# Optimization experiments

Hardware: AMD Instinct MI355X
Metric: run time of the kernel (lower is better)

## Reference

```python
import jax, jax.numpy as jnp
import numpy as np

N, B, L = 1000, 16, 12
H, IN_DIM, OUT_DIM, E = 64, 3, 1, 16000


def _gru_cell(x, h, Wi, Wh, bi, bh):
    # torch nn.GRU gate order: r, z, n
    gi = x @ Wi.T + bi
    gh = h @ Wh.T + bh
    ir, iz, inn = jnp.split(gi, 3, axis=-1)
    hr, hz, hn = jnp.split(gh, 3, axis=-1)
    r = jax.nn.sigmoid(ir + hr)
    z = jax.nn.sigmoid(iz + hz)
    n = jnp.tanh(inn + r * hn)
    return (1.0 - z) * n + z * h


def setup_inputs():
    key = jax.random.key(0)
    ks = jax.random.split(key, 24)
    def rn(k, shape, s=0.1):
        return jax.random.normal(k, shape, dtype=jnp.float32) * s
    return {
        "hidden0": rn(ks[0], (N, B, H), 1.0),
        "hidden1": rn(ks[1], (N, B, H), 1.0),
        "features": rn(ks[2], (N, H), 1.0),
        "labels": rn(ks[3], (N, B, L, IN_DIM), 1.0),
        "edge_index": jax.random.randint(ks[4], (2, E), 0, N),
        # GRU1: input_dim -> H
        "Wi1": rn(ks[5], (3 * H, IN_DIM)), "Wh1": rn(ks[6], (3 * H, H)),
        "bi1": rn(ks[7], (3 * H,)), "bh1": rn(ks[8], (3 * H,)),
        # MetaGAT MLP: 2H -> 16 -> 2 -> 2H*H
        "W1": rn(ks[9], (16, 2 * H)), "b1": rn(ks[10], (16,)),
        "W2": rn(ks[11], (2, 16)), "b2": rn(ks[12], (2,)),
        "W3": rn(ks[13], (2 * H * H, 2)), "b3": rn(ks[14], (2 * H * H,)),
        # GRU2: H -> H
        "Wi2": rn(ks[15], (3 * H, H)), "Wh2": rn(ks[16], (3 * H, H)),
        "bi2": rn(ks[17], (3 * H,)), "bh2": rn(ks[18], (3 * H,)),
        # output layer: 2H -> OUT_DIM
        "Wo": rn(ks[19], (OUT_DIM, 2 * H)), "bo": rn(ks[20], (OUT_DIM,)),
    }


def reference(hidden0, hidden1, features, labels, edge_index,
              Wi1, Wh1, bi1, bh1, W1, b1, W2, b2, W3, b3,
              Wi2, Wh2, bi2, bh2, Wo, bo):
    n, b, length, _ = labels.shape
    h = Wh1.shape[1]
    out_dim = Wo.shape[0]
    in_dim = Wi1.shape[1]
    aux = labels[..., out_dim:]  # [N,B,L,aux_dim]
    # add self loops (as in MetaGAT.forward)
    loops = jnp.arange(n)
    src = jnp.concatenate([edge_index[0], loops])  # j, source
    dst = jnp.concatenate([edge_index[1], loops])  # i, target
    # per-edge weight matrices; features are constant across timesteps so hoist
    ft = jnp.concatenate([features[dst], features[src]], axis=-1)  # [Etot,2H]
    w = jax.nn.sigmoid(ft @ W1.T + b1)
    w = jax.nn.sigmoid(w @ W2.T + b2)
    w = (w @ W3.T + b3).reshape(-1, 2 * h, h)  # [Etot,2H,H]
    feat_b = jnp.broadcast_to(features[:, None, :], (n, b, features.shape[-1]))

    def step(carry, idx):
        h0, h1, prev = carry
        aux_prev = jnp.take(aux, jnp.maximum(idx - 1, 0), axis=2)  # [N,B,aux]
        # eval path (train_mode=False): feed back previous prediction
        data = jnp.where(idx == 0,
                         jnp.zeros((n, b, in_dim), labels.dtype),
                         jnp.concatenate([prev, aux_prev], axis=-1))
        h0n = _gru_cell(data.reshape(n * b, in_dim), h0.reshape(n * b, h),
                        Wi1, Wh1, bi1, bh1).reshape(n, b, h)
        # MetaGAT message passing
        st_j = h0n[src]                                  # [Etot,B,H]
        st = jnp.concatenate([h0n[dst], st_j], axis=-1)  # [Etot,B,2H]
        alpha = jax.nn.leaky_relu(jnp.einsum('ebk,ekh->ebh', st, w), 0.01)
        alpha = jax.nn.softmax(alpha, axis=1)            # softmax over batch dim (faithful to source)
        agg = jax.ops.segment_sum(alpha * st_j, dst, num_segments=n)
        gat = jax.nn.relu(agg)                           # [N,B,H]
        h1n = _gru_cell(gat.reshape(n * b, h), h1.reshape(n * b, h),
                        Wi2, Wh2, bi2, bh2).reshape(n, b, h)
        pred = jnp.concatenate([h1n, feat_b], axis=-1) @ Wo.T + bo  # [N,B,out_dim]
        return (h0n, h1n, pred), pred

    init = (hidden0, hidden1, jnp.zeros((n, b, out_dim), labels.dtype))
    _, preds = jax.lax.scan(step, init, jnp.arange(length))
    return jnp.moveaxis(preds, 0, 2)  # [N,B,L,out_dim]
```

## Files before the change

### kernel.cpp

```cpp
#include <hip/hip_runtime.h>

#define N_NODES 1000
#define BATCH 16
#define SEQ 12
#define IN_DIM 3
#define HDIM 64
#define E_EDGES 16000
#define EN (E_EDGES + N_NODES)
#define NB (N_NODES * BATCH)

typedef unsigned int u32;
typedef unsigned short u16;

__device__ __forceinline__ float sigmoidf(float x) { return 1.0f / (1.0f + expf(-x)); }

__device__ __forceinline__ u16 f2bf(float x) {
    u32 u = __builtin_bit_cast(u32, x);
    u32 r = (u + 0x7fffu + ((u >> 16) & 1u)) >> 16;
    return (u16)r;
}
__device__ __forceinline__ float bf2f(u32 h) {
    return __builtin_bit_cast(float, (h & 0xffffu) << 16);
}
__device__ __forceinline__ u32 pack2(float a, float b) {
    return (u32)f2bf(a) | ((u32)f2bf(b) << 16);
}

__global__ void prep_kernel(const float* __restrict__ hidden0,
                            const float* __restrict__ hidden1,
                            const float* __restrict__ features,
                            const float* __restrict__ W3,
                            const float* __restrict__ b3,
                            const float* __restrict__ Wo,
                            const float* __restrict__ bo,
                            const float* __restrict__ Wh1,
                            const float* __restrict__ Wi1,
                            const float* __restrict__ Wi2,
                            const float* __restrict__ Wh2,
                            float* __restrict__ h0, float* __restrict__ h1,
                            float* __restrict__ M,
                            float* __restrict__ Wh1T, float* __restrict__ Wi1T,
                            float* __restrict__ Wi2T, float* __restrict__ Wh2T,
                            float* __restrict__ fpred, float* __restrict__ prev)
{
    int tid = blockIdx.x * blockDim.x + threadIdx.x;
    int stride = gridDim.x * blockDim.x;

    for (int i = tid; i < NB * HDIM; i += stride) { h0[i] = hidden0[i]; h1[i] = hidden1[i]; }

    for (int i = tid; i < 64 * 384; i += stride) {
        int k = i / 384, c = i % 384;
        int grp = c / 64, h = c % 64;
        int kk = (grp < 3 ? k : 64 + k) * 64 + h;
        float val;
        if (grp == 0 || grp == 3)      val = W3[kk * 2 + 0];
        else if (grp == 1 || grp == 4) val = W3[kk * 2 + 1];
        else                           val = b3[kk];
        M[i] = val;
    }

    for (int i = tid; i < 192 * 64; i += stride) {
        int k = i / 192, gj = i % 192;
        Wh1T[i] = Wh1[gj * 64 + k];
        Wi2T[i] = Wi2[gj * 64 + k];
        Wh2T[i] = Wh2[gj * 64 + k];
    }
    for (int i = tid; i < 3 * 192; i += stride) {
        int c = i / 192, gj = i % 192;
        Wi1T[i] = Wi1[gj * 3 + c];
    }

    for (int i = tid; i < NB; i += stride) prev[i] = 0.0f;

    for (int n = tid; n < N_NODES; n += stride) {
        float acc = bo[0];
        for (int h = 0; h < HDIM; ++h) acc += features[n * HDIM + h] * Wo[64 + h];
        fpred[n] = acc;
    }
}

__global__ void deg_init_kernel(int* __restrict__ deg)
{
    int n = blockIdx.x * blockDim.x + threadIdx.x;
    if (n < N_NODES) deg[n] = 1;
}

__global__ void deg_count_kernel(const int* __restrict__ edge_index, int* __restrict__ deg)
{
    int e = blockIdx.x * blockDim.x + threadIdx.x;
    if (e < E_EDGES) atomicAdd(&deg[edge_index[E_EDGES + e]], 1);
}

__global__ __launch_bounds__(1024) void scan_kernel(const int* __restrict__ deg,
                                                    int* __restrict__ row_ptr,
                                                    int* __restrict__ row_fill)
{
    __shared__ int s[1024];
    int tid = threadIdx.x;
    int x = (tid < N_NODES) ? deg[tid] : 0;
    s[tid] = x;
    __syncthreads();
    for (int off = 1; off < 1024; off <<= 1) {
        int v = (tid >= off) ? s[tid - off] : 0;
        __syncthreads();
        s[tid] += v;
        __syncthreads();
    }
    int incl = s[tid];
    int excl = incl - x;
    if (tid < N_NODES) { row_ptr[tid] = excl; row_fill[tid] = excl; }
    if (tid == N_NODES - 1) row_ptr[N_NODES] = incl;
}

__global__ void scatter_kernel(const int* __restrict__ edge_index,
                               int* __restrict__ row_fill,
                               int* __restrict__ csr_src,
                               int* __restrict__ perm)
{
    int e = blockIdx.x * blockDim.x + threadIdx.x;
    if (e < E_EDGES) {
        int s = edge_index[e];
        int d = edge_index[E_EDGES + e];
        int p = atomicAdd(&row_fill[d], 1);
        csr_src[p] = s;
        perm[e] = p;
    } else if (e < EN) {
        int n = e - E_EDGES;
        int p = atomicAdd(&row_fill[n], 1);
        csr_src[p] = n;
        perm[e] = p;
    }
}

__global__ __launch_bounds__(256) void edge_mlp_kernel(const int* __restrict__ edge_index,
                                                       const float* __restrict__ features,
                                                       const float* __restrict__ W1,
                                                       const float* __restrict__ b1,
                                                       const float* __restrict__ W2,
                                                       const float* __restrict__ b2,
                                                       const int* __restrict__ perm,
                                                       float* __restrict__ csr_uv)
{
    int w = threadIdx.x >> 6, j = threadIdx.x & 63;
    int e = blockIdx.x * 4 + w;
    int s, d;
    if (e < E_EDGES) { s = edge_index[e]; d = edge_index[E_EDGES + e]; }
    else             { s = e - E_EDGES; d = s; }

    __shared__ float ft[4][128];
    __shared__ float w1s[4][16];
    ft[w][j]      = features[d * HDIM + j];
    ft[w][64 + j] = features[s * HDIM + j];
    __syncthreads();

    int o = j & 15, part = j >> 4;
    float acc = 0.0f;
    #pragma unroll 8
    for (int kk = 0; kk < 32; ++kk)
        acc += ft[w][part * 32 + kk] * W1[o * 128 + part * 32 + kk];
    acc += __shfl_xor(acc, 16, 64);
    acc += __shfl_xor(acc, 32, 64);
    if (j < 16) w1s[w][j] = sigmoidf(acc + b1[j]);
    __syncthreads();
    if (j < 2) {
        float a2 = b2[j];
        #pragma unroll
        for (int k = 0; k < 16; ++k) a2 += w1s[w][k] * W2[j * 16 + k];
        csr_uv[perm[e] * 2 + j] = sigmoidf(a2);
    }
}

__global__ __launch_bounds__(256) void gru1_proj_kernel(const float* __restrict__ labels,
                                                        const float* __restrict__ prev,
                                                        const float* __restrict__ Wi1T,
                                                        const float* __restrict__ Wh1T,
                                                        const float* __restrict__ bi1,
                                                        const float* __restrict__ bh1,
                                                        const float* __restrict__ M,
                                                        float* __restrict__ h0,
                                                        uint2* __restrict__ Pd,
                                                        uint2* __restrict__ Ps,
                                                        int t)
{
    int w = threadIdx.x >> 6, j = threadIdx.x & 63;
    int rbase = blockIdx.x * 32 + w * 8;
    __shared__ float hs[32][64];

    #pragma unroll
    for (int rr = 0; rr < 8; ++rr)
        hs[w * 8 + rr][j] = h0[(size_t)(rbase + rr) * HDIM + j];

    float ar[8], az[8], an[8];
    {
        float br = bh1[j], bz = bh1[64 + j], bn = bh1[128 + j];
        #pragma unroll
        for (int rr = 0; rr < 8; ++rr) { ar[rr] = br; az[rr] = bz; an[rr] = bn; }
    }

    for (int k = 0; k < 64; k += 2) {
        const float* w0 = &Wh1T[(size_t)k * 192 + j];
        float wr0 = w0[0], wz0 = w0[64], wn0 = w0[128];
        float wr1 = w0[192], wz1 = w0[256], wn1 = w0[320];
        #pragma unroll
        for (int rr = 0; rr < 8; ++rr) {
            float2 h2 = *(const float2*)&hs[w * 8 + rr][k];
            ar[rr] = fmaf(wr0, h2.x, ar[rr]);
            az[rr] = fmaf(wz0, h2.x, az[rr]);
            an[rr] = fmaf(wn0, h2.x, an[rr]);
            ar[rr] = fmaf(wr1, h2.y, ar[rr]);
            az[rr] = fmaf(wz1, h2.y, az[rr]);
            an[rr] = fmaf(wn1, h2.y, an[rr]);
        }
    }

    float wi00 = Wi1T[j],       wi01 = Wi1T[64 + j],       wi02 = Wi1T[128 + j];
    float wi10 = Wi1T[192 + j], wi11 = Wi1T[192 + 64 + j], wi12 = Wi1T[192 + 128 + j];
    float wi20 = Wi1T[384 + j], wi21 = Wi1T[384 + 64 + j], wi22 = Wi1T[384 + 128 + j];
    float bir = bi1[j], biz = bi1[64 + j], bin_ = bi1[128 + j];

    #pragma unroll
    for (int rr = 0; rr < 8; ++rr) {
        int row = rbase + rr;
        float x0 = 0.f, x1 = 0.f, x2 = 0.f;
        if (t > 0) {
            x0 = prev[row];
            const float* lab = labels + ((size_t)row * SEQ + (t - 1)) * IN_DIM;
            x1 = lab[1]; x2 = lab[2];
        }
        float gir = bir  + x0 * wi00 + x1 * wi10 + x2 * wi20;
        float giz = biz  + x0 * wi01 + x1 * wi11 + x2 * wi21;
        float gin = bin_ + x0 * wi02 + x1 * wi12 + x2 * wi22;
        float rg = sigmoidf(gir + ar[rr]);
        float zg = sigmoidf(giz + az[rr]);
        float ng = tanhf(gin + rg * an[rr]);
        float hj = hs[w * 8 + rr][j];
        float hn = (1.0f - zg) * ng + zg * hj;
        h0[(size_t)row * HDIM + j] = hn;
        hs[w * 8 + rr][j] = hn;
    }

    float a0[8], a1[8], a2[8], a3[8], a4[8], a5[8];
    #pragma unroll
    for (int rr = 0; rr < 8; ++rr) { a0[rr]=0.f; a1[rr]=0.f; a2[rr]=0.f; a3[rr]=0.f; a4[rr]=0.f; a5[rr]=0.f; }

    for (int k = 0; k < 64; ++k) {
        const float* mrow = &M[(size_t)k * 384 + j];
        float m0 = mrow[0],   m1 = mrow[64],  m2 = mrow[128];
        float m3 = mrow[192], m4 = mrow[256], m5 = mrow[320];
        #pragma unroll
        for (int rr = 0; rr < 8; ++rr) {
            float hk = hs[w * 8 + rr][k];
            a0[rr] = fmaf(m0, hk, a0[rr]); a1[rr] = fmaf(m1, hk, a1[rr]);
            a2[rr] = fmaf(m2, hk, a2[rr]); a3[rr] = fmaf(m3, hk, a3[rr]);
            a4[rr] = fmaf(m4, hk, a4[rr]); a5[rr] = fmaf(m5, hk, a5[rr]);
        }
    }

    #pragma unroll
    for (int rr = 0; rr < 8; ++rr) {
        size_t row = rbase + rr;
        float stj = hs[w * 8 + rr][j];
        Pd[row * 64 + j] = make_uint2(pack2(a0[rr], a1[rr]), pack2(a2[rr], 0.f));
        Ps[row * 64 + j] = make_uint2(pack2(a3[rr], a4[rr]), pack2(a5[rr], stj));
    }
}

__global__ __launch_bounds__(256) void edge_step_kernel(const int* __restrict__ row_ptr,
                                                        const int* __restrict__ csr_src,
                                                        const float* __restrict__ csr_uv,
                                                        const uint2* __restrict__ Pd,
                                                        const uint2* __restrict__ Ps,
                                                        float* __restrict__ agg)
{
    int d = blockIdx.x;
    int w = threadIdx.x >> 6, h = threadIdx.x & 63;

    uint2 pdreg[BATCH];
    #pragma unroll
    for (int b = 0; b < BATCH; ++b)
        pdreg[b] = Pd[((size_t)d * BATCH + b) * 64 + h];

    float acc[BATCH];
    #pragma unroll
    for (int b = 0; b < BATCH; ++b) acc[b] = 0.0f;

    int start = row_ptr[d], end = row_ptr[d + 1];
    for (int p = start + w; p < end; p += 4) {
        int s = csr_src[p];
        float u = csr_uv[p * 2], v = csr_uv[p * 2 + 1];

        float al[BATCH], stj[BATCH];
        #pragma unroll
        for (int b = 0; b < BATCH; ++b) {
            uint2 pd = pdreg[b];
            uint2 ps = Ps[((size_t)s * BATCH + b) * 64 + h];
            float c0 = bf2f(pd.x), c1 = bf2f(pd.x >> 16), c2 = bf2f(pd.y);
            float c3 = bf2f(ps.x), c4 = bf2f(ps.x >> 16), c5 = bf2f(ps.y);
            float a = u * (c0 + c3) + v * (c1 + c4) + c2 + c5;
            al[b] = (a > 0.0f) ? a : 0.01f * a;
            stj[b] = bf2f(ps.y >> 16);
        }
        float m = al[0];
        #pragma unroll
        for (int b = 1; b < BATCH; ++b) m = fmaxf(m, al[b]);
        float sum = 0.0f;
        #pragma unroll
        for (int b = 0; b < BATCH; ++b) { al[b] = expf(al[b] - m); sum += al[b]; }
        float inv = 1.0f / sum;
        #pragma unroll
        for (int b = 0; b < BATCH; ++b) acc[b] = fmaf(al[b] * inv, stj[b], acc[b]);
    }

    __shared__ float red[4][BATCH][HDIM];
    #pragma unroll
    for (int b = 0; b < BATCH; ++b) red[w][b][h] = acc[b];
    __syncthreads();

    for (int c = threadIdx.x; c < BATCH * HDIM; c += 256) {
        float s4 = red[0][0][c] + red[1][0][c] + red[2][0][c] + red[3][0][c];
        agg[(size_t)d * BATCH * HDIM + c] = s4;
    }
}

__global__ __launch_bounds__(256) void gru2_pred_kernel(const float* __restrict__ agg,
                                                        const float* __restrict__ Wi2T,
                                                        const float* __restrict__ Wh2T,
                                                        const float* __restrict__ bi2,
                                                        const float* __restrict__ bh2,
                                                        const float* __restrict__ Wo,
                                                        const float* __restrict__ fpred,
                                                        float* __restrict__ h1,
                                                        float* __restrict__ prev,
                                                        float* __restrict__ out,
                                                        int t)
{
    int w = threadIdx.x >> 6, j = threadIdx.x & 63;
    int rbase = blockIdx.x * 32 + w * 8;
    __shared__ float gs[32][64];
    __shared__ float hs[32][64];

    #pragma unroll
    for (int rr = 0; rr < 8; ++rr) {
        float g = agg[(size_t)(rbase + rr) * HDIM + j];
        gs[w * 8 + rr][j] = fmaxf(g, 0.0f);
        hs[w * 8 + rr][j] = h1[(size_t)(rbase + rr) * HDIM + j];
    }

    float acr[8], acz[8], ain[8], ahn[8];
    {
        float b0 = bi2[j] + bh2[j], b1 = bi2[64 + j] + bh2[64 + j];
        float b2 = bi2[128 + j], c2 = bh2[128 + j];
        #pragma unroll
        for (int rr = 0; rr < 8; ++rr) { acr[rr] = b0; acz[rr] = b1; ain[rr] = b2; ahn[rr] = c2; }
    }

    for (int k = 0; k < 64; ++k) {
        const float* wiRow = &Wi2T[(size_t)k * 192 + j];
        const float* whRow = &Wh2T[(size_t)k * 192 + j];
        float wir = wiRow[0], wiz = wiRow[64], win = wiRow[128];
        float whr = whRow[0], whz = whRow[64], whn = whRow[128];
        #pragma unroll
        for (int rr = 0; rr < 8; ++rr) {
            float gk = gs[w * 8 + rr][k];
            float hk = hs[w * 8 + rr][k];
            acr[rr] = fmaf(wir, gk, acr[rr]);  acr[rr] = fmaf(whr, hk, acr[rr]);
            acz[rr] = fmaf(wiz, gk, acz[rr]);  acz[rr] = fmaf(whz, hk, acz[rr]);
            ain[rr] = fmaf(win, gk, ain[rr]);  ahn[rr] = fmaf(whn, hk, ahn[rr]);
        }
    }

    float woj = Wo[j];
    #pragma unroll
    for (int rr = 0; rr < 8; ++rr) {
        float rg = sigmoidf(acr[rr]);
        float zg = sigmoidf(acz[rr]);
        float ng = tanhf(ain[rr] + rg * ahn[rr]);
        float hj = hs[w * 8 + rr][j];
        float hn = (1.0f - zg) * ng + zg * hj;
        h1[(size_t)(rbase + rr) * HDIM + j] = hn;

        float part = hn * woj;
        #pragma unroll
        for (int off = 32; off; off >>= 1) part += __shfl_xor(part, off, 64);
        if (j == rr) {
            int row = rbase + rr;
            float p = part + fpred[row / BATCH];
            prev[row] = p;
            out[(size_t)row * SEQ + t] = p;
        }
    }
}

extern "C" void kernel_launch(void* const* d_in, const int* in_sizes, int n_in,
                              void* d_out, int out_size, void* d_ws, size_t ws_size,
                              hipStream_t stream)
{
    const float* hidden0  = (const float*)d_in[0];
    const float* hidden1  = (const float*)d_in[1];
    const float* features = (const float*)d_in[2];
    const float* labels   = (const float*)d_in[3];
    const int*   edge_idx = (const int*)d_in[4];
    const float* Wi1 = (const float*)d_in[5];
    const float* Wh1 = (const float*)d_in[6];
    const float* bi1 = (const float*)d_in[7];
    const float* bh1 = (const float*)d_in[8];
    const float* W1  = (const float*)d_in[9];
    const float* b1  = (const float*)d_in[10];
    const float* W2  = (const float*)d_in[11];
    const float* b2  = (const float*)d_in[12];
    const float* W3  = (const float*)d_in[13];
    const float* b3  = (const float*)d_in[14];
    const float* Wi2 = (const float*)d_in[15];
    const float* Wh2 = (const float*)d_in[16];
    const float* bi2 = (const float*)d_in[17];
    const float* bh2 = (const float*)d_in[18];
    const float* Wo  = (const float*)d_in[19];
    const float* bo  = (const float*)d_in[20];

    float* ws = (float*)d_ws;
    float* h0    = ws;  ws += NB * HDIM;
    float* h1    = ws;  ws += NB * HDIM;
    uint2* Pd    = (uint2*)ws;  ws += NB * HDIM * 2;
    uint2* Ps    = (uint2*)ws;  ws += NB * HDIM * 2;
    float* agg   = ws;  ws += NB * HDIM;
    float* csr_uv= ws;  ws += EN * 2;
    float* M     = ws;  ws += 64 * 384;
    float* Wh1T  = ws;  ws += 64 * 192;
    float* Wi1T  = ws;  ws += 3 * 192;
    float* Wi2T  = ws;  ws += 64 * 192;
    float* Wh2T  = ws;  ws += 64 * 192;
    float* fpred = ws;  ws += N_NODES;
    float* prev  = ws;  ws += NB;
    int*   deg      = (int*)ws;  ws += N_NODES;
    int*   row_ptr  = (int*)ws;  ws += N_NODES + 1;
    int*   row_fill = (int*)ws;  ws += N_NODES;
    int*   csr_src  = (int*)ws;  ws += EN;
    int*   perm     = (int*)ws;  ws += EN;
    float* out   = (float*)d_out;

    prep_kernel<<<256, 256, 0, stream>>>(hidden0, hidden1, features, W3, b3, Wo, bo,
                                         Wh1, Wi1, Wi2, Wh2,
                                         h0, h1, M, Wh1T, Wi1T, Wi2T, Wh2T, fpred, prev);
    deg_init_kernel<<<(N_NODES + 255) / 256, 256, 0, stream>>>(deg);
    deg_count_kernel<<<(E_EDGES + 255) / 256, 256, 0, stream>>>(edge_idx, deg);
    scan_kernel<<<1, 1024, 0, stream>>>(deg, row_ptr, row_fill);
    scatter_kernel<<<(EN + 255) / 256, 256, 0, stream>>>(edge_idx, row_fill, csr_src, perm);
    edge_mlp_kernel<<<(EN + 3) / 4, 256, 0, stream>>>(edge_idx, features, W1, b1, W2, b2,
                                                      perm, csr_uv);

    for (int t = 0; t < SEQ; ++t) {
        gru1_proj_kernel<<<NB / 32, 256, 0, stream>>>(labels, prev, Wi1T, Wh1T, bi1, bh1,
                                                      M, h0, Pd, Ps, t);
        edge_step_kernel<<<N_NODES, 256, 0, stream>>>(row_ptr, csr_src, csr_uv, Pd, Ps, agg);
        gru2_pred_kernel<<<NB / 32, 256, 0, stream>>>(agg, Wi2T, Wh2T, bi2, bh2, Wo, fpred,
                                                      h1, prev, out, t);
    }
}
```

Before: 993.9 us.

## Fuse edge aggregation and GRU2/prediction into one per-node kernel

Merges the edge attention-aggregation kernel and the GRU2+output kernel into a single kernel with one block per destination node. The aggregated messages stay in shared memory instead of passing through a global agg buffer, which saves one launch and one global write/read per timestep. In exchange, each block's GRU2 matmul now covers only 16 rows (4 per wave), so each weight load is reused half as much, and the shared-memory footprint per block grows.

```diff
diff --git a/kernel.cpp b/kernel.cpp
--- a/kernel.cpp
+++ b/kernel.cpp
@@ -265,64 +265,11 @@
     }
 }
 
-__global__ __launch_bounds__(256) void edge_step_kernel(const int* __restrict__ row_ptr,
+__global__ __launch_bounds__(256) void edge_gru2_kernel(const int* __restrict__ row_ptr,
                                                         const int* __restrict__ csr_src,
                                                         const float* __restrict__ csr_uv,
                                                         const uint2* __restrict__ Pd,
                                                         const uint2* __restrict__ Ps,
-                                                        float* __restrict__ agg)
-{
-    int d = blockIdx.x;
-    int w = threadIdx.x >> 6, h = threadIdx.x & 63;
-
-    uint2 pdreg[BATCH];
-    #pragma unroll
-    for (int b = 0; b < BATCH; ++b)
-        pdreg[b] = Pd[((size_t)d * BATCH + b) * 64 + h];
-
-    float acc[BATCH];
-    #pragma unroll
-    for (int b = 0; b < BATCH; ++b) acc[b] = 0.0f;
-
-    int start = row_ptr[d], end = row_ptr[d + 1];
-    for (int p = start + w; p < end; p += 4) {
-        int s = csr_src[p];
-        float u = csr_uv[p * 2], v = csr_uv[p * 2 + 1];
-
-        float al[BATCH], stj[BATCH];
-        #pragma unroll
-        for (int b = 0; b < BATCH; ++b) {
-            uint2 pd = pdreg[b];
-            uint2 ps = Ps[((size_t)s * BATCH + b) * 64 + h];
-            float c0 = bf2f(pd.x), c1 = bf2f(pd.x >> 16), c2 = bf2f(pd.y);
-            float c3 = bf2f(ps.x), c4 = bf2f(ps.x >> 16), c5 = bf2f(ps.y);
-            float a = u * (c0 + c3) + v * (c1 + c4) + c2 + c5;
-            al[b] = (a > 0.0f) ? a : 0.01f * a;
-            stj[b] = bf2f(ps.y >> 16);
-        }
-        float m = al[0];
-        #pragma unroll
-        for (int b = 1; b < BATCH; ++b) m = fmaxf(m, al[b]);
-        float sum = 0.0f;
-        #pragma unroll
-        for (int b = 0; b < BATCH; ++b) { al[b] = expf(al[b] - m); sum += al[b]; }
-        float inv = 1.0f / sum;
-        #pragma unroll
-        for (int b = 0; b < BATCH; ++b) acc[b] = fmaf(al[b] * inv, stj[b], acc[b]);
-    }
-
-    __shared__ float red[4][BATCH][HDIM];
-    #pragma unroll
-    for (int b = 0; b < BATCH; ++b) red[w][b][h] = acc[b];
-    __syncthreads();
-
-    for (int c = threadIdx.x; c < BATCH * HDIM; c += 256) {
-        float s4 = red[0][0][c] + red[1][0][c] + red[2][0][c] + red[3][0][c];
-        agg[(size_t)d * BATCH * HDIM + c] = s4;
-    }
-}
-
-__global__ __launch_bounds__(256) void gru2_pred_kernel(const float* __restrict__ agg,
                                                         const float* __restrict__ Wi2T,
                                                         const float* __restrict__ Wh2T,
                                                         const float* __restrict__ bi2,
@@ -334,24 +281,69 @@
                                                         float* __restrict__ out,
                                                         int t)
 {
+    int d = blockIdx.x;
     int w = threadIdx.x >> 6, j = threadIdx.x & 63;
-    int rbase = blockIdx.x * 32 + w * 8;
-    __shared__ float gs[32][64];
-    __shared__ float hs[32][64];
-
-    #pragma unroll
-    for (int rr = 0; rr < 8; ++rr) {
-        float g = agg[(size_t)(rbase + rr) * HDIM + j];
-        gs[w * 8 + rr][j] = fmaxf(g, 0.0f);
-        hs[w * 8 + rr][j] = h1[(size_t)(rbase + rr) * HDIM + j];
-    }
-
-    float acr[8], acz[8], ain[8], ahn[8];
+
+    __shared__ float red[4][BATCH][HDIM];
+    __shared__ float gs[BATCH][HDIM];
+    __shared__ float hs[BATCH][HDIM];
+
+    #pragma unroll
+    for (int rr = 0; rr < 4; ++rr)
+        hs[w * 4 + rr][j] = h1[(size_t)(d * BATCH + w * 4 + rr) * HDIM + j];
+
+    uint2 pdreg[BATCH];
+    #pragma unroll
+    for (int b = 0; b < BATCH; ++b)
+        pdreg[b] = Pd[((size_t)d * BATCH + b) * 64 + j];
+
+    float acc[BATCH];
+    #pragma unroll
+    for (int b = 0; b < BATCH; ++b) acc[b] = 0.0f;
+
+    int start = row_ptr[d], end = row_ptr[d + 1];
+    for (int p = start + w; p < end; p += 4) {
+        int s = csr_src[p];
+        float u = csr_uv[p * 2], v = csr_uv[p * 2 + 1];
+
+        float al[BATCH], stj[BATCH];
+        #pragma unroll
+        for (int b = 0; b < BATCH; ++b) {
+            uint2 pd = pdreg[b];
+            uint2 ps = Ps[((size_t)s * BATCH + b) * 64 + j];
+            float a = u * (bf2f(pd.x) + bf2f(ps.x))
+                    + v * (bf2f(pd.x >> 16) + bf2f(ps.x >> 16))
+                    + bf2f(pd.y) + bf2f(ps.y);
+            al[b] = (a > 0.0f) ? a : 0.01f * a;
+            stj[b] = bf2f(ps.y >> 16);
+        }
+        float m = al[0];
+        #pragma unroll
+        for (int b = 1; b < BATCH; ++b) m = fmaxf(m, al[b]);
+        float sum = 0.0f;
+        #pragma unroll
+        for (int b = 0; b < BATCH; ++b) { al[b] = expf(al[b] - m); sum += al[b]; }
+        float inv = 1.0f / sum;
+        #pragma unroll
+        for (int b = 0; b < BATCH; ++b) acc[b] = fmaf(al[b] * inv, stj[b], acc[b]);
+    }
+
+    #pragma unroll
+    for (int b = 0; b < BATCH; ++b) red[w][b][j] = acc[b];
+    __syncthreads();
+
+    for (int c = threadIdx.x; c < BATCH * HDIM; c += 256) {
+        float s4 = red[0][0][c] + red[1][0][c] + red[2][0][c] + red[3][0][c];
+        gs[0][c] = fmaxf(s4, 0.0f);
+    }
+    __syncthreads();
+
+    float acr[4], acz[4], ain[4], ahn[4];
     {
         float b0 = bi2[j] + bh2[j], b1 = bi2[64 + j] + bh2[64 + j];
         float b2 = bi2[128 + j], c2 = bh2[128 + j];
         #pragma unroll
-        for (int rr = 0; rr < 8; ++rr) { acr[rr] = b0; acz[rr] = b1; ain[rr] = b2; ahn[rr] = c2; }
+        for (int rr = 0; rr < 4; ++rr) { acr[rr] = b0; acz[rr] = b1; ain[rr] = b2; ahn[rr] = c2; }
     }
 
     for (int k = 0; k < 64; ++k) {
@@ -360,9 +352,9 @@
         float wir = wiRow[0], wiz = wiRow[64], win = wiRow[128];
         float whr = whRow[0], whz = whRow[64], whn = whRow[128];
         #pragma unroll
-        for (int rr = 0; rr < 8; ++rr) {
-            float gk = gs[w * 8 + rr][k];
-            float hk = hs[w * 8 + rr][k];
+        for (int rr = 0; rr < 4; ++rr) {
+            float gk = gs[w * 4 + rr][k];
+            float hk = hs[w * 4 + rr][k];
             acr[rr] = fmaf(wir, gk, acr[rr]);  acr[rr] = fmaf(whr, hk, acr[rr]);
             acz[rr] = fmaf(wiz, gk, acz[rr]);  acz[rr] = fmaf(whz, hk, acz[rr]);
             ain[rr] = fmaf(win, gk, ain[rr]);  ahn[rr] = fmaf(whn, hk, ahn[rr]);
@@ -370,21 +362,22 @@
     }
 
     float woj = Wo[j];
-    #pragma unroll
-    for (int rr = 0; rr < 8; ++rr) {
+    float fp = fpred[d];
+    #pragma unroll
+    for (int rr = 0; rr < 4; ++rr) {
+        int row = d * BATCH + w * 4 + rr;
         float rg = sigmoidf(acr[rr]);
         float zg = sigmoidf(acz[rr]);
         float ng = tanhf(ain[rr] + rg * ahn[rr]);
-        float hj = hs[w * 8 + rr][j];
+        float hj = hs[w * 4 + rr][j];
         float hn = (1.0f - zg) * ng + zg * hj;
-        h1[(size_t)(rbase + rr) * HDIM + j] = hn;
+        h1[(size_t)row * HDIM + j] = hn;
 
         float part = hn * woj;
         #pragma unroll
         for (int off = 32; off; off >>= 1) part += __shfl_xor(part, off, 64);
         if (j == rr) {
-            int row = rbase + rr;
-            float p = part + fpred[row / BATCH];
+            float p = part + fp;
             prev[row] = p;
             out[(size_t)row * SEQ + t] = p;
         }
@@ -422,7 +415,6 @@
     float* h1    = ws;  ws += NB * HDIM;
     uint2* Pd    = (uint2*)ws;  ws += NB * HDIM * 2;
     uint2* Ps    = (uint2*)ws;  ws += NB * HDIM * 2;
-    float* agg   = ws;  ws += NB * HDIM;
     float* csr_uv= ws;  ws += EN * 2;
     float* M     = ws;  ws += 64 * 384;
     float* Wh1T  = ws;  ws += 64 * 192;
@@ -451,8 +443,8 @@
     for (int t = 0; t < SEQ; ++t) {
         gru1_proj_kernel<<<NB / 32, 256, 0, stream>>>(labels, prev, Wi1T, Wh1T, bi1, bh1,
                                                       M, h0, Pd, Ps, t);
-        edge_step_kernel<<<N_NODES, 256, 0, stream>>>(row_ptr, csr_src, csr_uv, Pd, Ps, agg);
-        gru2_pred_kernel<<<NB / 32, 256, 0, stream>>>(agg, Wi2T, Wh2T, bi2, bh2, Wo, fpred,
+        edge_gru2_kernel<<<N_NODES, 256, 0, stream>>>(row_ptr, csr_src, csr_uv, Pd, Ps,
+                                                      Wi2T, Wh2T, bi2, bh2, Wo, fpred,
                                                       h1, prev, out, t);
     }
 }
```

Result: slower. 1.067 ms (+7.4%).
